# Optimization experiments

Hardware: AMD Instinct MI355X
Metric: run time of the kernel (lower is better)

## Reference

```python
import jax, jax.numpy as jnp
import numpy as np

# CT parallel-beam geometry (pixel-unit spacing, image-centered)
H = 512        # nImgY
W = 512        # nImgX
NVIEW = 768    # number of projection angles over [0, pi)
NDCT = 736     # detector bins (nDctX)
NT = 725       # samples along each ray ~ ceil(512*sqrt(2))


def setup_inputs() -> dict:
    key = jax.random.key(0)
    # [B, C, H, W] image volume (C = nslice slices)
    x = jax.random.uniform(key, (1, 2, H, W), dtype=jnp.float32)
    return {"input": x}


def _bilinear(img, ix, iy):
    """Bilinear sample img [C,H,W] at float pixel coords ix,iy [D,T] with zero padding.
    Returns [C,D,T]."""
    x0 = jnp.floor(ix)
    y0 = jnp.floor(iy)
    wx = ix - x0
    wy = iy - y0
    x0i = x0.astype(jnp.int32)
    y0i = y0.astype(jnp.int32)

    def gather(yi, xi):
        valid = (xi >= 0) & (xi < W) & (yi >= 0) & (yi < H)
        xc = jnp.clip(xi, 0, W - 1)
        yc = jnp.clip(yi, 0, H - 1)
        v = img[:, yc, xc]                      # [C,D,T]
        return jnp.where(valid, v, jnp.float32(0.0))

    v00 = gather(y0i, x0i)
    v01 = gather(y0i, x0i + 1)
    v10 = gather(y0i + 1, x0i)
    v11 = gather(y0i + 1, x0i + 1)
    return (v00 * (1 - wx) * (1 - wy) + v01 * wx * (1 - wy)
            + v10 * (1 - wx) * wy + v11 * wx * wy)


def _radon(img):
    """Parallel-beam Radon transform: img [C,H,W] -> sinogram [C,NVIEW,NDCT]."""
    s = jnp.arange(NDCT, dtype=jnp.float32) - (NDCT - 1) / 2.0   # detector coords
    t = jnp.arange(NT, dtype=jnp.float32) - (NT - 1) / 2.0       # along-ray coords
    cx = (W - 1) / 2.0
    cy = (H - 1) / 2.0
    thetas = jnp.arange(NVIEW, dtype=jnp.float32) * jnp.float32(np.pi / NVIEW)

    def step(_, th):
        c, sn = jnp.cos(th), jnp.sin(th)
        # sample points of each (detector, ray-step) pair, image-centered coords
        x = s[:, None] * c - t[None, :] * sn + cx   # [NDCT,NT]
        y = s[:, None] * sn + t[None, :] * c + cy
        vals = _bilinear(img, x, y)                  # [C,NDCT,NT]
        return None, vals.sum(-1)                    # line integral -> [C,NDCT]

    _, proj = jax.lax.scan(step, None, thetas)       # [NVIEW,C,NDCT]
    return jnp.transpose(proj, (1, 0, 2))            # [C,NVIEW,NDCT]


def reference(input) -> jnp.ndarray:
    B, C, Hh, Ww = input.shape
    img = input.reshape(B * C, Hh, Ww)               # module reshapes to (-1,1,H,W)
    proj = _radon(img)                               # [B*C,NVIEW,NDCT]
    return proj.reshape(B, C, NVIEW, NDCT)
```

## Files before the change

kernel.cpp:

```cpp
#include <hip/hip_runtime.h>
#include <hip/hip_fp16.h>

typedef float v2f __attribute__((ext_vector_type(2)));

#define IMG_H 512
#define IMG_W 512
#define NVIEW 768
#define NDCT 736
#define NT 725
#define PAD 2
#define PW (IMG_W + 2 * PAD)
#define PH (IMG_H + 2 * PAD)
#define TROWS 20
#define TCOLS 132
#define LSTR 160
#define VCHUNK 16

__global__ void repack_kernel(const float* __restrict__ in,
                              __half2* __restrict__ packed,
                              __half2* __restrict__ packedT) {
    int i = blockIdx.x * blockDim.x + threadIdx.x;
    if (i < PH * PW) {
        int py = i / PW;
        int px = i - py * PW;
        int y = py - PAD;
        int x = px - PAD;
        float2 v = make_float2(0.0f, 0.0f);
        if ((unsigned)x < (unsigned)IMG_W && (unsigned)y < (unsigned)IMG_H) {
            v = make_float2(in[y * IMG_W + x], in[IMG_H * IMG_W + y * IMG_W + x]);
        }
        __half2 h = __floats2half2_rn(v.x, v.y);
        packed[py * PW + px] = h;
        packedT[px * PW + py] = h;
    }
}

__device__ __forceinline__ void lsamp(const __half2* __restrict__ lds, v2f pos, v2f& acc) {
    float fx = floorf(pos.x);
    float fy = floorf(pos.y);
    int xi = (int)fx;
    int yi = (int)fy;
    float wx = pos.x - fx;
    float wy = pos.y - fy;
    int idx = yi * LSTR + xi;
    __half2 v00 = lds[idx];
    __half2 v01 = lds[idx + 1];
    __half2 v10 = lds[idx + LSTR];
    __half2 v11 = lds[idx + LSTR + 1];
    __half2 hwx = __float2half2_rn(wx);
    __half2 hwy = __float2half2_rn(wy);
    __half2 top = __hfma2(hwx, __hsub2(v01, v00), v00);
    __half2 bot = __hfma2(hwx, __hsub2(v11, v10), v10);
    __half2 smp = __hfma2(hwy, __hsub2(bot, top), top);
    acc += (v2f){__low2float(smp), __high2float(smp)};
}

__global__ __launch_bounds__(512, 8) void radon_tile_kernel(const __half2* __restrict__ packed,
                                                            const __half2* __restrict__ packedT,
                                                            float* __restrict__ out) {
    __shared__ __half2 lds[TROWS * LSTR];

    const int tid = threadIdx.x;
    const int bx = blockIdx.x;
    const int by = blockIdx.y;
    const bool classA = (by < 12) || (by >= 36);

    int x0, y0;
    float xlo, xhi, ylo, yhi;
    if (classA) {
        int tx = bx & 3, ty = bx >> 2;
        x0 = tx * 128; y0 = ty * 16;
        xlo = (tx == 0) ? -1.25f : (float)x0;
        xhi = (tx == 3) ? 512.25f : (float)(x0 + 128);
        ylo = (ty == 0) ? -1.25f : (float)y0;
        yhi = (ty == 31) ? 512.25f : (float)(y0 + 16);
    } else {
        int tx = bx & 31, ty = bx >> 5;
        x0 = tx * 16; y0 = ty * 128;
        xlo = (tx == 0) ? -1.25f : (float)x0;
        xhi = (tx == 31) ? 512.25f : (float)(x0 + 16);
        ylo = (ty == 0) ? -1.25f : (float)y0;
        yhi = (ty == 3) ? 512.25f : (float)(y0 + 128);
    }

    {
        const __half2* src = classA ? packed : packedT;
        const int rbase = classA ? y0 : x0;
        const int cbase = classA ? x0 : y0;
        for (int i = tid; i < TROWS * TCOLS; i += 512) {
            int r = i / TCOLS;
            int cc = i - r * TCOLS;
            lds[r * LSTR + cc] = src[(rbase + r) * PW + (cbase + cc)];
        }
    }
    __syncthreads();

    const int wid = tid >> 6;
    const int lane = tid & 63;
    const float cx = 255.5f;
    const float doff = 367.5f;
    const float T0 = -362.0f;
    const float x0f = (float)x0, y0f = (float)y0;
    const int vbase = by * VCHUNK;

    for (int task = wid; task < 2 * VCHUNK; task += 8) {
        const int view = vbase + (task >> 1);
        const int half = task & 1;
        const float theta = (float)view * (float)(3.14159265358979323846 / (double)NVIEW);
        float sn, c;
        sincosf(theta, &sn, &c);

        float xa = c * (xlo - cx), xb = c * (xhi - cx);
        float ya = sn * (ylo - cx), yb = sn * (yhi - cx);
        float smin = fminf(xa, xb) + fminf(ya, yb) - 1.0f;
        float smax = fmaxf(xa, xb) + fmaxf(ya, yb) + 1.0f;
        int detlo = max(0, (int)ceilf(smin + doff));
        int dethi = min(NDCT - 1, (int)floorf(smax + doff));

        if (detlo + (half << 6) > dethi) continue;

        auto do_ray = [&](int det) {
            bool active = (det <= dethi);
            float s = (float)det - doff;
            float sx = fmaf(s, c, cx);
            float sy = fmaf(s, sn, cx);

            float tlo = T0 - 1.0f, thi = -T0;
            const float eps = 1e-7f;
            if (sn > eps) {
                float r = __frcp_rn(sn);
                tlo = fmaxf(tlo, (sx - xhi) * r);
                thi = fminf(thi, (sx - xlo) * r);
            } else if (sx < xlo || sx >= xhi) {
                active = false;
            }
            if (c > eps) {
                float r = __frcp_rn(c);
                tlo = fmaxf(tlo, (ylo - sy) * r);
                thi = fminf(thi, (yhi - sy) * r);
            } else if (c < -eps) {
                float r = __frcp_rn(c);
                tlo = fmaxf(tlo, (yhi - sy) * r);
                thi = fminf(thi, (ylo - sy) * r);
            } else if (sy < ylo || sy >= yhi) {
                active = false;
            }

            float a = fmaxf(fminf(tlo - T0, 726.0f), -2.0f);
            float b = fmaxf(fminf(thi - T0, 724.0f), -3.0f);
            int tt0 = max(0, (int)floorf(a) + 1);
            int tt1 = (int)floorf(b);
            if (!active) tt1 = tt0 - 1;
            int n = tt1 - tt0 + 1;

            float t0f = (float)tt0 + T0;
            float xs = fmaf(t0f, -sn, sx) - x0f + 2.0f;
            float ys = fmaf(t0f, c, sy) - y0f + 2.0f;
            v2f pos, stp;
            if (classA) { pos = (v2f){xs, ys}; stp = (v2f){-sn, c}; }
            else        { pos = (v2f){ys, xs}; stp = (v2f){c, -sn}; }

            v2f acc0 = {0.0f, 0.0f}, acc1 = {0.0f, 0.0f};
            v2f stp2 = stp + stp;
            int k = n;
            while (k >= 2) {
                v2f p1 = pos + stp;
                lsamp(lds, pos, acc0);
                lsamp(lds, p1, acc1);
                pos += stp2;
                k -= 2;
            }
            if (k == 1) lsamp(lds, pos, acc0);
            v2f acc = acc0 + acc1;

            if (n > 0) {
                atomicAdd(&out[view * NDCT + det], acc.x);
                atomicAdd(&out[NVIEW * NDCT + view * NDCT + det], acc.y);
            }
        };

        do_ray(detlo + (half << 6) + lane);
        if (half == 1 && detlo + 128 <= dethi) do_ray(detlo + 128 + lane);
    }
}

extern "C" void kernel_launch(void* const* d_in, const int* in_sizes, int n_in,
                              void* d_out, int out_size, void* d_ws, size_t ws_size,
                              hipStream_t stream) {
    const float* in = (const float*)d_in[0];
    float* out = (float*)d_out;
    __half2* packed = (__half2*)d_ws;
    __half2* packedT = packed + PW * PH;

    hipMemsetAsync(d_out, 0, (size_t)out_size * sizeof(float), stream);

    {
        int n = PH * PW;
        int threads = 256;
        int blocks = (n + threads - 1) / threads;
        repack_kernel<<<blocks, threads, 0, stream>>>(in, packed, packedT);
    }
    {
        dim3 block(512, 1, 1);
        dim3 grid(128, NVIEW / VCHUNK, 1);
        radon_tile_kernel<<<grid, block, 0, stream>>>(packed, packedT, out);
    }
}
```

Before: 258.0 us.

## Pack vertical pixel pairs in LDS and accumulate ray sums in half precision

Each LDS entry now holds a pixel together with the pixel one row below it, so each bilinear sample needs two 8-byte LDS loads instead of four 4-byte loads. Per-ray accumulation also moves from float to packed half2 adds, removing the per-sample half-to-float conversions. This doubles LDS footprint per block, which may reduce occupancy. Accumulating up to ~128 samples per ray in fp16 risks precision loss against the float reference.

```diff
diff --git a/kernel.cpp b/kernel.cpp
--- a/kernel.cpp
+++ b/kernel.cpp
@@ -15,6 +15,8 @@
 #define TCOLS 132
 #define LSTR 160
 #define VCHUNK 16
+
+typedef struct { __half2 a, b; } h2x2;
 
 __global__ void repack_kernel(const float* __restrict__ in,
                               __half2* __restrict__ packed,
@@ -35,7 +37,7 @@
     }
 }
 
-__device__ __forceinline__ void lsamp(const __half2* __restrict__ lds, v2f pos, v2f& acc) {
+__device__ __forceinline__ void lsamp(const h2x2* __restrict__ lds, v2f pos, __half2& acc) {
     float fx = floorf(pos.x);
     float fy = floorf(pos.y);
     int xi = (int)fx;
@@ -43,22 +45,19 @@
     float wx = pos.x - fx;
     float wy = pos.y - fy;
     int idx = yi * LSTR + xi;
-    __half2 v00 = lds[idx];
-    __half2 v01 = lds[idx + 1];
-    __half2 v10 = lds[idx + LSTR];
-    __half2 v11 = lds[idx + LSTR + 1];
+    h2x2 L = lds[idx];
+    h2x2 R = lds[idx + 1];
     __half2 hwx = __float2half2_rn(wx);
     __half2 hwy = __float2half2_rn(wy);
-    __half2 top = __hfma2(hwx, __hsub2(v01, v00), v00);
-    __half2 bot = __hfma2(hwx, __hsub2(v11, v10), v10);
-    __half2 smp = __hfma2(hwy, __hsub2(bot, top), top);
-    acc += (v2f){__low2float(smp), __high2float(smp)};
+    __half2 top = __hfma2(hwx, __hsub2(R.a, L.a), L.a);
+    __half2 bot = __hfma2(hwx, __hsub2(R.b, L.b), L.b);
+    acc = __hadd2(acc, __hfma2(hwy, __hsub2(bot, top), top));
 }
 
 __global__ __launch_bounds__(512, 8) void radon_tile_kernel(const __half2* __restrict__ packed,
                                                             const __half2* __restrict__ packedT,
                                                             float* __restrict__ out) {
-    __shared__ __half2 lds[TROWS * LSTR];
+    __shared__ h2x2 lds[TROWS * LSTR];
 
     const int tid = threadIdx.x;
     const int bx = blockIdx.x;
@@ -90,7 +89,12 @@
         for (int i = tid; i < TROWS * TCOLS; i += 512) {
             int r = i / TCOLS;
             int cc = i - r * TCOLS;
-            lds[r * LSTR + cc] = src[(rbase + r) * PW + (cbase + cc)];
+            int gr = rbase + r;
+            int gr2 = min(gr + 1, PH - 1);
+            h2x2 e;
+            e.a = src[gr * PW + cbase + cc];
+            e.b = src[gr2 * PW + cbase + cc];
+            lds[r * LSTR + cc] = e;
         }
     }
     __syncthreads();
@@ -160,22 +164,23 @@
             if (classA) { pos = (v2f){xs, ys}; stp = (v2f){-sn, c}; }
             else        { pos = (v2f){ys, xs}; stp = (v2f){c, -sn}; }
 
-            v2f acc0 = {0.0f, 0.0f}, acc1 = {0.0f, 0.0f};
+            __half2 hacc0 = __floats2half2_rn(0.0f, 0.0f);
+            __half2 hacc1 = __floats2half2_rn(0.0f, 0.0f);
             v2f stp2 = stp + stp;
             int k = n;
             while (k >= 2) {
                 v2f p1 = pos + stp;
-                lsamp(lds, pos, acc0);
-                lsamp(lds, p1, acc1);
+                lsamp(lds, pos, hacc0);
+                lsamp(lds, p1, hacc1);
                 pos += stp2;
                 k -= 2;
             }
-            if (k == 1) lsamp(lds, pos, acc0);
-            v2f acc = acc0 + acc1;
+            if (k == 1) lsamp(lds, pos, hacc0);
+            __half2 hs = __hadd2(hacc0, hacc1);
 
             if (n > 0) {
-                atomicAdd(&out[view * NDCT + det], acc.x);
-                atomicAdd(&out[NVIEW * NDCT + view * NDCT + det], acc.y);
+                atomicAdd(&out[view * NDCT + det], __low2float(hs));
+                atomicAdd(&out[NVIEW * NDCT + view * NDCT + det], __high2float(hs));
             }
         };
 
```

Result: faster. 243.5 us (-5.6%).
